# Optimization experiments

Measured on AMD Instinct MI355X. Metric: run time of the kernel, lower is better.

The kernel has to match this reference:

```python
import jax, jax.numpy as jnp
import numpy as np

S, B, D, H, DFF = 1024, 8, 1024, 16, 4096
HD = D // H
EPS = 1e-5


def layernorm(x, g, b):
    m = jnp.mean(x, axis=-1, keepdims=True)
    v = jnp.mean(jnp.square(x - m), axis=-1, keepdims=True)
    return (x - m) * jax.lax.rsqrt(v + EPS) * g + b


def setup_inputs() -> dict:
    key = jax.random.key(0)
    ks = jax.random.split(key, 6)
    w = 0.02
    return {
        "src": jax.random.normal(ks[0], (S, B, D), dtype=jnp.float32),
        "in_proj_w": jax.random.normal(ks[1], (3 * D, D), dtype=jnp.float32) * w,
        "in_proj_b": jnp.zeros((3 * D,), dtype=jnp.float32),
        "out_w": jax.random.normal(ks[2], (D, D), dtype=jnp.float32) * w,
        "out_b": jnp.zeros((D,), dtype=jnp.float32),
        "lin1_w": jax.random.normal(ks[3], (DFF, D), dtype=jnp.float32) * w,
        "lin1_b": jnp.zeros((DFF,), dtype=jnp.float32),
        "lin2_w": jax.random.normal(ks[4], (D, DFF), dtype=jnp.float32) * w,
        "lin2_b": jnp.zeros((D,), dtype=jnp.float32),
        "n1_g": jnp.ones((D,), dtype=jnp.float32),
        "n1_b": jnp.zeros((D,), dtype=jnp.float32),
        "n2_g": jnp.ones((D,), dtype=jnp.float32),
        "n2_b": jnp.zeros((D,), dtype=jnp.float32),
    }


def reference(src, in_proj_w, in_proj_b, out_w, out_b,
              lin1_w, lin1_b, lin2_w, lin2_b,
              n1_g, n1_b, n2_g, n2_b):
    # self-attention block (eval mode: dropout = identity)
    qkv = jnp.einsum('sbd,ed->sbe', src, in_proj_w) + in_proj_b  # [S,B,3D]
    q, k, v = jnp.split(qkv, 3, axis=-1)
    q = q.reshape(S, B, H, HD) * (1.0 / np.sqrt(HD)).astype(np.float32)
    k = k.reshape(S, B, H, HD)
    v = v.reshape(S, B, H, HD)
    scores = jnp.einsum('sbhd,tbhd->bhst', q, k)        # [B,H,S,S]
    attn = jax.nn.softmax(scores, axis=-1)
    o = jnp.einsum('bhst,tbhd->sbhd', attn, v).reshape(S, B, D)
    o = jnp.einsum('sbd,ed->sbe', o, out_w) + out_b
    # post-LN residuals
    x = layernorm(src + o, n1_g, n1_b)
    h = jax.nn.relu(jnp.einsum('sbd,fd->sbf', x, lin1_w) + lin1_b)
    f = jnp.einsum('sbf,df->sbd', h, lin2_w) + lin2_b
    return layernorm(x + f, n2_g, n2_b)
```

## Files before the change

### kernel.cpp

```cpp
#include <hip/hip_runtime.h>
#include <cstdint>
#include <cstddef>

#define S_  1024
#define B_  8
#define D_  1024
#define H_  16
#define HD_ 64
#define DFF_ 4096
#define M_  (S_*B_)
#define QKV_N (3*D_)

typedef float f32x4 __attribute__((ext_vector_type(4)));
typedef __bf16 bf16x8 __attribute__((ext_vector_type(8)));
typedef __bf16 bf16x4 __attribute__((ext_vector_type(4)));

#define GLDS16(gp, lp) __builtin_amdgcn_global_load_lds( \
    (__attribute__((address_space(1))) void*)(gp), \
    (__attribute__((address_space(3))) void*)(lp), 16, 0, 0)

#define CB0 (M_*D_/4)
#define CB1 (CB0 + QKV_N*D_/4)
#define CB2 (CB1 + D_*D_/4)
#define CB3 (CB2 + DFF_*D_/4)
#define CB4 (CB3 + D_*DFF_/4)

__global__ __launch_bounds__(256)
void cvt_all(const float* __restrict__ src, const float* __restrict__ w1f,
             const float* __restrict__ w2f, const float* __restrict__ w3f,
             const float* __restrict__ w4f,
             __bf16* __restrict__ src_bf, __bf16* __restrict__ w1,
             __bf16* __restrict__ w2, __bf16* __restrict__ w3,
             __bf16* __restrict__ w4)
{
    int i = blockIdx.x * 256 + threadIdx.x;
    const float* in; __bf16* out; int off;
    if      (i < CB0) { in = src; out = src_bf; off = 0;   }
    else if (i < CB1) { in = w1f; out = w1;     off = CB0; }
    else if (i < CB2) { in = w2f; out = w2;     off = CB1; }
    else if (i < CB3) { in = w3f; out = w3;     off = CB2; }
    else if (i < CB4) { in = w4f; out = w4;     off = CB3; }
    else return;
    int j = i - off;
    float4 v = *(const float4*)(in + (size_t)j * 4);
    __bf16 t[4] = {(__bf16)v.x, (__bf16)v.y, (__bf16)v.z, (__bf16)v.w};
    *(uint2*)(out + (size_t)j * 4) = *(uint2*)t;
}

template<bool OUT_BF16, bool RELU, bool ADD_BIAS, bool SPLITZ>
__global__ __launch_bounds__(512, 2)
void gemm256(const __bf16* __restrict__ A, const __bf16* __restrict__ W,
             const float* __restrict__ bias,
             void* __restrict__ Cv0, void* __restrict__ Cv1,
             int N, int Kloop, int lda)
{
    extern __shared__ __bf16 lds[];
    __bf16* As = lds;
    __bf16* Bs = lds + 3 * 8192;

    const int tid  = threadIdx.x;
    const int lane = tid & 63;
    const int wv   = tid >> 6;
    const int quad = lane >> 4;
    const int l15  = lane & 15;
    const int wm   = (wv >> 2) * 128;
    const int wn   = (wv & 3) * 64;

    const int id  = blockIdx.y * gridDim.x + blockIdx.x;
    const int nwg = gridDim.x * gridDim.y;
    const int q8  = nwg >> 3;
    const int k   = (id & 7) * q8 + (id >> 3);
    const int within = k & 31;
    const int chunk  = k >> 5;
    const int nchm   = gridDim.x >> 3;
    const int cm     = chunk % nchm;
    const int cn     = chunk / nchm;
    const int m0 = (cm * 8 + (within & 7)) * 256;
    const int n0 = (cn * 4 + (within >> 3)) * 256;

    void* Cv = Cv0;
    if (SPLITZ) {
        const int koff = blockIdx.z * Kloop;
        A += koff;
        W += koff;
        if (blockIdx.z) Cv = Cv1;
    }

    const int nt = Kloop >> 5;

    #define STAGE(kt, buf) do { \
        const int k0s = (kt) << 5; \
        _Pragma("unroll") \
        for (int u = 0; u < 2; ++u) { \
            int c   = u * 512 + tid; \
            int row = c >> 2; \
            int ssl = (c & 3) ^ ((row >> 1) & 3); \
            GLDS16(A + (size_t)(m0 + row) * lda + k0s + ssl * 8, \
                   (char*)(As + (buf) * 8192) + c * 16); \
            GLDS16(W + (size_t)(n0 + row) * lda + k0s + ssl * 8, \
                   (char*)(Bs + (buf) * 8192) + c * 16); \
        } \
    } while (0)

    STAGE(0, 0);
    STAGE(1, 1);
    asm volatile("s_waitcnt vmcnt(4)" ::: "memory");
    __builtin_amdgcn_s_barrier();
    __builtin_amdgcn_sched_barrier(0);

    f32x4 acc[8][4] = {};

    int cur = 0, stg = 2;
    for (int t = 0; t < nt; ++t) {
        if (t + 2 < nt) STAGE(t + 2, stg);

        bf16x8 bf[4], af[8];
        #pragma unroll
        for (int j = 0; j < 4; ++j) {
            int rb = wn + j * 16 + l15;
            bf[j] = *(const bf16x8*)(Bs + cur * 8192 + rb * 32 + (quad ^ ((rb >> 1) & 3)) * 8);
        }
        #pragma unroll
        for (int i = 0; i < 8; ++i) {
            int ra = wm + i * 16 + l15;
            af[i] = *(const bf16x8*)(As + cur * 8192 + ra * 32 + (quad ^ ((ra >> 1) & 3)) * 8);
        }

        __builtin_amdgcn_s_setprio(1);
        #pragma unroll
        for (int i = 0; i < 8; ++i)
            #pragma unroll
            for (int j = 0; j < 4; ++j)
                acc[i][j] = __builtin_amdgcn_mfma_f32_16x16x32_bf16(af[i], bf[j], acc[i][j], 0, 0, 0);
        __builtin_amdgcn_s_setprio(0);

        if (t + 1 < nt) {
            if (t + 2 < nt) { asm volatile("s_waitcnt vmcnt(4)" ::: "memory"); }
            else            { asm volatile("s_waitcnt vmcnt(0)" ::: "memory"); }
            __builtin_amdgcn_s_barrier();
            __builtin_amdgcn_sched_barrier(0);
        }
        if (++cur == 3) cur = 0;
        if (++stg == 3) stg = 0;
    }
    #undef STAGE

    float bvj[4];
    #pragma unroll
    for (int j = 0; j < 4; ++j)
        bvj[j] = ADD_BIAS ? bias[n0 + wn + j * 16 + l15] : 0.f;
    #pragma unroll
    for (int i = 0; i < 8; ++i) {
        const int rbase = m0 + wm + i * 16 + quad * 4;
        #pragma unroll
        for (int r = 0; r < 4; ++r) {
            #pragma unroll
            for (int j = 0; j < 4; ++j) {
                const int col = n0 + wn + j * 16 + l15;
                float v = acc[i][j][r] + bvj[j];
                if (RELU) v = fmaxf(v, 0.f);
                if (OUT_BF16)
                    ((__bf16*)Cv)[(size_t)(rbase + r) * N + col] = (__bf16)v;
                else
                    ((float*)Cv)[(size_t)(rbase + r) * N + col] = v;
            }
        }
    }
}

__global__ __launch_bounds__(256)
void v_transpose(const __bf16* __restrict__ qkv, __bf16* __restrict__ vt)
{
    __shared__ __bf16 T[64 * 65];
    const int tid = threadIdx.x;
    const int t0  = blockIdx.x * 64;
    const int bh  = blockIdx.y;
    const int b   = bh & (B_ - 1);
    const int h   = bh / B_;

    #pragma unroll
    for (int j = 0; j < 2; ++j) {
        int c = j * 256 + tid;
        int i = c >> 3, cc = c & 7;
        const __bf16* g = qkv + (size_t)((t0 + i) * B_ + b) * QKV_N + 2 * D_ + h * HD_ + cc * 8;
        bf16x8 v = *(const bf16x8*)g;
        #pragma unroll
        for (int u = 0; u < 8; ++u) T[(cc * 8 + u) * 65 + i] = v[u];
    }
    __syncthreads();
    #pragma unroll
    for (int j = 0; j < 2; ++j) {
        int c = j * 256 + tid;
        int d = c >> 3, cc = c & 7;
        __bf16 pk[8];
        #pragma unroll
        for (int u = 0; u < 8; ++u) pk[u] = T[d * 65 + cc * 8 + u];
        *(uint4*)(vt + ((size_t)bh * HD_ + d) * S_ + t0 + cc * 8) = *(uint4*)pk;
    }
}

#define TST 72

__global__ __launch_bounds__(256)
void attn_flash(const __bf16* __restrict__ qkv, const __bf16* __restrict__ vt,
                __bf16* __restrict__ out)
{
    __shared__ __bf16 Qs[64 * TST];
    __shared__ __bf16 Ks[64 * TST];
    __shared__ __bf16 Vt[64 * TST];
    __shared__ __bf16 Ps[64 * TST];

    const int tid  = threadIdx.x;
    const int lane = tid & 63;
    const int wv   = tid >> 6;
    const int quad = lane >> 4;
    const int l15  = lane & 15;

    const int id = blockIdx.y * gridDim.x + blockIdx.x;
    const int k  = (id & 7) * ((S_ / 64) * B_ * H_ / 8) + (id >> 3);
    const int s0 = (k & 15) * 64;
    const int bh = k >> 4;
    const int b  = bh & (B_ - 1);
    const int h  = bh / B_;

    #pragma unroll
    for (int j = 0; j < 2; ++j) {
        int c = j * 256 + tid;
        int i = c >> 3, cc = c & 7;
        const __bf16* g = qkv + (size_t)((s0 + i) * B_ + b) * QKV_N + h * HD_ + cc * 8;
        *(uint4*)(Qs + i * TST + cc * 8) = *(const uint4*)g;
    }

    f32x4 oacc[4] = {};
    float m_run = -1e30f, l_run = 0.f;
    const float C2    = 0.125f * 1.44269504f;
    const float LOG2E = 1.44269504f;

    for (int t0 = 0; t0 < S_; t0 += 64) {
        __syncthreads();
        #pragma unroll
        for (int j = 0; j < 2; ++j) {
            int c = j * 256 + tid;
            int i = c >> 3, cc = c & 7;
            const __bf16* g = qkv + (size_t)((t0 + i) * B_ + b) * QKV_N + D_ + h * HD_ + cc * 8;
            *(uint4*)(Ks + i * TST + cc * 8) = *(const uint4*)g;
        }
        #pragma unroll
        for (int j = 0; j < 2; ++j) {
            int c = j * 256 + tid;
            int d = c >> 3, cc = c & 7;
            const __bf16* g = vt + ((size_t)bh * HD_ + d) * S_ + t0 + cc * 8;
            *(uint4*)(Vt + d * TST + cc * 8) = *(const uint4*)g;
        }
        __syncthreads();

        f32x4 sacc[4] = {};
        #pragma unroll
        for (int kk = 0; kk < 2; ++kk) {
            bf16x8 bq = *(const bf16x8*)(Qs + (wv * 16 + l15) * TST + kk * 32 + quad * 8);
            #pragma unroll
            for (int j = 0; j < 4; ++j) {
                bf16x8 ak = *(const bf16x8*)(Ks + (j * 16 + l15) * TST + kk * 32 + quad * 8);
                sacc[j] = __builtin_amdgcn_mfma_f32_16x16x32_bf16(ak, bq, sacc[j], 0, 0, 0);
            }
        }

        float mx = sacc[0][0];
        #pragma unroll
        for (int j = 0; j < 4; ++j)
            #pragma unroll
            for (int r = 0; r < 4; ++r) mx = fmaxf(mx, sacc[j][r]);
        mx = fmaxf(mx, __shfl_xor(mx, 16, 64));
        mx = fmaxf(mx, __shfl_xor(mx, 32, 64));
        float mnew = fmaxf(m_run, mx * 0.125f);
        float k1 = mnew * LOG2E;
        float rs = 0.f;
        #pragma unroll
        for (int j = 0; j < 4; ++j)
            #pragma unroll
            for (int r = 0; r < 4; ++r) {
                float p = __builtin_amdgcn_exp2f(sacc[j][r] * C2 - k1);
                sacc[j][r] = p;
                rs += p;
            }
        rs += __shfl_xor(rs, 16, 64);
        rs += __shfl_xor(rs, 32, 64);
        float alpha = __builtin_amdgcn_exp2f((m_run - mnew) * LOG2E);
        l_run = l_run * alpha + rs;
        m_run = mnew;

        #pragma unroll
        for (int j = 0; j < 4; ++j) {
            __bf16 pk[4] = {(__bf16)sacc[j][0], (__bf16)sacc[j][1],
                            (__bf16)sacc[j][2], (__bf16)sacc[j][3]};
            *(uint2*)(Ps + (wv * 16 + l15) * TST + j * 16 + quad * 4) = *(uint2*)pk;
        }

        #pragma unroll
        for (int r = 0; r < 4; ++r) {
            float ar = __shfl(alpha, quad * 4 + r, 64);
            #pragma unroll
            for (int jd = 0; jd < 4; ++jd) oacc[jd][r] *= ar;
        }

        #pragma unroll
        for (int kk = 0; kk < 2; ++kk) {
            bf16x8 ap = *(const bf16x8*)(Ps + (wv * 16 + l15) * TST + kk * 32 + quad * 8);
            #pragma unroll
            for (int jd = 0; jd < 4; ++jd) {
                bf16x8 bv = *(const bf16x8*)(Vt + (jd * 16 + l15) * TST + kk * 32 + quad * 8);
                oacc[jd] = __builtin_amdgcn_mfma_f32_16x16x32_bf16(ap, bv, oacc[jd], 0, 0, 0);
            }
        }
    }

    float linv = 1.f / l_run;
    #pragma unroll
    for (int r = 0; r < 4; ++r) {
        float lr = __shfl(linv, quad * 4 + r, 64);
        int s = s0 + wv * 16 + quad * 4 + r;
        #pragma unroll
        for (int jd = 0; jd < 4; ++jd) {
            int d = jd * 16 + l15;
            out[(size_t)(s * B_ + b) * D_ + h * HD_ + d] = (__bf16)(oacc[jd][r] * lr);
        }
    }
}

__global__ __launch_bounds__(256)
void ln_res3(const float* __restrict__ xa, const __bf16* __restrict__ p0,
             const __bf16* __restrict__ p1, const float* __restrict__ bias,
             const float* __restrict__ g, const float* __restrict__ beta,
             float* __restrict__ yout, __bf16* __restrict__ ybf)
{
    __shared__ float red[8];
    const int row = blockIdx.x;
    const int tid = threadIdx.x;
    const size_t base = (size_t)row * D_ + tid * 4;

    float4 a  = *(const float4*)(xa + base);
    bf16x4 q0 = *(const bf16x4*)(p0 + base);
    bf16x4 q1 = *(const bf16x4*)(p1 + base);
    float4 bb = *(const float4*)(bias + tid * 4);
    float x0 = a.x + (float)q0[0] + (float)q1[0] + bb.x;
    float x1 = a.y + (float)q0[1] + (float)q1[1] + bb.y;
    float x2 = a.z + (float)q0[2] + (float)q1[2] + bb.z;
    float x3 = a.w + (float)q0[3] + (float)q1[3] + bb.w;

    float s  = x0 + x1 + x2 + x3;
    float ss = x0 * x0 + x1 * x1 + x2 * x2 + x3 * x3;
    for (int msk = 1; msk <= 32; msk <<= 1) {
        s  += __shfl_xor(s,  msk, 64);
        ss += __shfl_xor(ss, msk, 64);
    }
    const int wv = tid >> 6;
    if ((tid & 63) == 0) { red[wv] = s; red[4 + wv] = ss; }
    __syncthreads();
    s  = red[0] + red[1] + red[2] + red[3];
    ss = red[4] + red[5] + red[6] + red[7];
    float mean = s * (1.f / D_);
    float var  = ss * (1.f / D_) - mean * mean;
    float rstd = rsqrtf(var + 1e-5f);

    float4 gv = *(const float4*)(g + tid * 4);
    float4 bv = *(const float4*)(beta + tid * 4);
    float y0 = (x0 - mean) * rstd * gv.x + bv.x;
    float y1 = (x1 - mean) * rstd * gv.y + bv.y;
    float y2 = (x2 - mean) * rstd * gv.z + bv.z;
    float y3 = (x3 - mean) * rstd * gv.w + bv.w;
    *(float4*)(yout + base) = make_float4(y0, y1, y2, y3);
    if (ybf) {
        __bf16 t[4] = {(__bf16)y0, (__bf16)y1, (__bf16)y2, (__bf16)y3};
        *(uint2*)(ybf + base) = *(uint2*)t;
    }
}

extern "C" void kernel_launch(void* const* d_in, const int* in_sizes, int n_in,
                              void* d_out, int out_size, void* d_ws, size_t ws_size,
                              hipStream_t stream)
{
    const float* src       = (const float*)d_in[0];
    const float* in_proj_w = (const float*)d_in[1];
    const float* in_proj_b = (const float*)d_in[2];
    const float* out_w     = (const float*)d_in[3];
    const float* out_b     = (const float*)d_in[4];
    const float* lin1_w    = (const float*)d_in[5];
    const float* lin1_b    = (const float*)d_in[6];
    const float* lin2_w    = (const float*)d_in[7];
    const float* lin2_b    = (const float*)d_in[8];
    const float* n1_g = (const float*)d_in[9];
    const float* n1_b = (const float*)d_in[10];
    const float* n2_g = (const float*)d_in[11];
    const float* n2_b = (const float*)d_in[12];

    char* ws = (char*)d_ws;
    size_t off = 0;
    auto alloc = [&](size_t bytes) { char* p = ws + off; off += (bytes + 255) & ~(size_t)255; return p; };

    __bf16* src_bf = (__bf16*)alloc((size_t)M_ * D_ * 2);
    __bf16* w1     = (__bf16*)alloc((size_t)QKV_N * D_ * 2);
    __bf16* w2     = (__bf16*)alloc((size_t)D_ * D_ * 2);
    __bf16* w3     = (__bf16*)alloc((size_t)DFF_ * D_ * 2);
    __bf16* w4     = (__bf16*)alloc((size_t)D_ * DFF_ * 2);
    __bf16* qkv    = (__bf16*)alloc((size_t)M_ * QKV_N * 2);
    char*   h_r    = alloc((size_t)M_ * DFF_ * 2);
    __bf16* xbf    = (__bf16*)alloc((size_t)M_ * D_ * 2);
    float*  xf     = (float*)alloc((size_t)M_ * D_ * 4);
    __bf16* vt     = (__bf16*)alloc((size_t)B_ * H_ * HD_ * S_ * 2);

    const size_t PART = (size_t)M_ * D_;
    __bf16* attn_o = src_bf;
    __bf16* o0 = (__bf16*)h_r;
    __bf16* o1 = o0 + PART;
    __bf16* hbf = (__bf16*)h_r;
    __bf16* f0 = vt;
    __bf16* f1 = xbf;

    const size_t SHM = 3 * 2 * 8192 * sizeof(__bf16);

    cvt_all<<<(CB4 + 255) / 256, 256, 0, stream>>>(
        src, in_proj_w, out_w, lin1_w, lin2_w, src_bf, w1, w2, w3, w4);

    gemm256<true, false, true, false><<<dim3(M_ / 256, QKV_N / 256), 512, SHM, stream>>>(
        src_bf, w1, in_proj_b, qkv, nullptr, QKV_N, D_, D_);

    v_transpose<<<dim3(S_ / 64, B_ * H_), 256, 0, stream>>>(qkv, vt);

    attn_flash<<<dim3(S_ / 64, B_ * H_), 256, 0, stream>>>(qkv, vt, attn_o);

    gemm256<true, false, false, true><<<dim3(M_ / 256, D_ / 256, 2), 512, SHM, stream>>>(
        attn_o, w2, nullptr, o0, o1, D_, D_ / 2, D_);

    ln_res3<<<M_, 256, 0, stream>>>(src, o0, o1, out_b, n1_g, n1_b, xf, xbf);

    gemm256<true, true, true, false><<<dim3(M_ / 256, DFF_ / 256), 512, SHM, stream>>>(
        xbf, w3, lin1_b, hbf, nullptr, DFF_, D_, D_);

    gemm256<true, false, false, true><<<dim3(M_ / 256, D_ / 256, 2), 512, SHM, stream>>>(
        hbf, w4, nullptr, f0, f1, D_, DFF_ / 2, DFF_);

    ln_res3<<<M_, 256, 0, stream>>>(xf, f0, f1, lin2_b, n2_g, n2_b, (float*)d_out, nullptr);
}
```

Baseline: 495.7 us.

## Prefetch next K/V tile into registers and XOR-swizzle attention LDS tiles

The flash-attention kernel now loads the next K and V tile from global memory into registers while the current tile's MFMAs run, then writes them to LDS at the top of the next iteration. This hides global load latency behind compute. It also replaces the padded LDS stride (72) with an unpadded stride of 64 and an XOR swizzle on 16-byte chunks, which keeps bank conflicts low while using less LDS. The cost is extra registers for the prefetch buffers, which may lower occupancy. The barrier also moves from the start of the loop to its end.

```diff
diff --git a/kernel.cpp b/kernel.cpp
--- a/kernel.cpp
+++ b/kernel.cpp
@@ -199,16 +199,16 @@
     }
 }
 
-#define TST 72
+#define AST 64
 
 __global__ __launch_bounds__(256)
 void attn_flash(const __bf16* __restrict__ qkv, const __bf16* __restrict__ vt,
                 __bf16* __restrict__ out)
 {
-    __shared__ __bf16 Qs[64 * TST];
-    __shared__ __bf16 Ks[64 * TST];
-    __shared__ __bf16 Vt[64 * TST];
-    __shared__ __bf16 Ps[64 * TST];
+    __shared__ __bf16 Qs[64 * AST];
+    __shared__ __bf16 Ks[64 * AST];
+    __shared__ __bf16 Vt[64 * AST];
+    __shared__ __bf16 Ps[64 * AST];
 
     const int tid  = threadIdx.x;
     const int lane = tid & 63;
@@ -228,7 +228,16 @@
         int c = j * 256 + tid;
         int i = c >> 3, cc = c & 7;
         const __bf16* g = qkv + (size_t)((s0 + i) * B_ + b) * QKV_N + h * HD_ + cc * 8;
-        *(uint4*)(Qs + i * TST + cc * 8) = *(const uint4*)g;
+        *(uint4*)(Qs + i * AST + ((cc ^ (i & 7)) * 8)) = *(const uint4*)g;
+    }
+
+    uint4 kreg[2], vreg[2];
+    #pragma unroll
+    for (int j = 0; j < 2; ++j) {
+        int c = j * 256 + tid;
+        int i = c >> 3, cc = c & 7;
+        kreg[j] = *(const uint4*)(qkv + (size_t)((i) * B_ + b) * QKV_N + D_ + h * HD_ + cc * 8);
+        vreg[j] = *(const uint4*)(vt + ((size_t)bh * HD_ + i) * S_ + cc * 8);
     }
 
     f32x4 oacc[4] = {};
@@ -237,30 +246,35 @@
     const float LOG2E = 1.44269504f;
 
     for (int t0 = 0; t0 < S_; t0 += 64) {
-        __syncthreads();
         #pragma unroll
         for (int j = 0; j < 2; ++j) {
             int c = j * 256 + tid;
             int i = c >> 3, cc = c & 7;
-            const __bf16* g = qkv + (size_t)((t0 + i) * B_ + b) * QKV_N + D_ + h * HD_ + cc * 8;
-            *(uint4*)(Ks + i * TST + cc * 8) = *(const uint4*)g;
-        }
-        #pragma unroll
-        for (int j = 0; j < 2; ++j) {
-            int c = j * 256 + tid;
-            int d = c >> 3, cc = c & 7;
-            const __bf16* g = vt + ((size_t)bh * HD_ + d) * S_ + t0 + cc * 8;
-            *(uint4*)(Vt + d * TST + cc * 8) = *(const uint4*)g;
+            *(uint4*)(Ks + i * AST + ((cc ^ (i & 7)) * 8)) = kreg[j];
+            *(uint4*)(Vt + i * AST + ((cc ^ (i & 7)) * 8)) = vreg[j];
         }
         __syncthreads();
 
+        if (t0 + 64 < S_) {
+            const int t1 = t0 + 64;
+            #pragma unroll
+            for (int j = 0; j < 2; ++j) {
+                int c = j * 256 + tid;
+                int i = c >> 3, cc = c & 7;
+                kreg[j] = *(const uint4*)(qkv + (size_t)((t1 + i) * B_ + b) * QKV_N + D_ + h * HD_ + cc * 8);
+                vreg[j] = *(const uint4*)(vt + ((size_t)bh * HD_ + i) * S_ + t1 + cc * 8);
+            }
+        }
+
         f32x4 sacc[4] = {};
+        const int qrow = wv * 16 + l15;
         #pragma unroll
         for (int kk = 0; kk < 2; ++kk) {
-            bf16x8 bq = *(const bf16x8*)(Qs + (wv * 16 + l15) * TST + kk * 32 + quad * 8);
+            bf16x8 bq = *(const bf16x8*)(Qs + qrow * AST + (((kk * 4 + quad) ^ (qrow & 7)) * 8));
             #pragma unroll
             for (int j = 0; j < 4; ++j) {
-                bf16x8 ak = *(const bf16x8*)(Ks + (j * 16 + l15) * TST + kk * 32 + quad * 8);
+                int krow = j * 16 + l15;
+                bf16x8 ak = *(const bf16x8*)(Ks + krow * AST + (((kk * 4 + quad) ^ (krow & 7)) * 8));
                 sacc[j] = __builtin_amdgcn_mfma_f32_16x16x32_bf16(ak, bq, sacc[j], 0, 0, 0);
             }
         }
@@ -293,7 +307,8 @@
         for (int j = 0; j < 4; ++j) {
             __bf16 pk[4] = {(__bf16)sacc[j][0], (__bf16)sacc[j][1],
                             (__bf16)sacc[j][2], (__bf16)sacc[j][3]};
-            *(uint2*)(Ps + (wv * 16 + l15) * TST + j * 16 + quad * 4) = *(uint2*)pk;
+            int s16 = (j * 2 + (quad >> 1)) ^ (qrow & 7);
+            *(uint2*)(Ps + qrow * AST + s16 * 8 + (quad & 1) * 4) = *(uint2*)pk;
         }
 
         #pragma unroll
@@ -305,13 +320,15 @@
 
         #pragma unroll
         for (int kk = 0; kk < 2; ++kk) {
-            bf16x8 ap = *(const bf16x8*)(Ps + (wv * 16 + l15) * TST + kk * 32 + quad * 8);
+            bf16x8 ap = *(const bf16x8*)(Ps + qrow * AST + (((kk * 4 + quad) ^ (qrow & 7)) * 8));
             #pragma unroll
             for (int jd = 0; jd < 4; ++jd) {
-                bf16x8 bv = *(const bf16x8*)(Vt + (jd * 16 + l15) * TST + kk * 32 + quad * 8);
+                int vrow = jd * 16 + l15;
+                bf16x8 bv = *(const bf16x8*)(Vt + vrow * AST + (((kk * 4 + quad) ^ (vrow & 7)) * 8));
                 oacc[jd] = __builtin_amdgcn_mfma_f32_16x16x32_bf16(ap, bv, oacc[jd], 0, 0, 0);
             }
         }
+        __syncthreads();
     }
 
     float linv = 1.f / l_run;
```

New measurement: 552.3 us. 11.4% more time.
